# Performance work log

Hardware: AMD Instinct MI355X
Metric: run time of the kernel (lower is better)

Reference implementation:

```python
import jax, jax.numpy as jnp
import numpy as np

N_NODES = 50000
HIDDEN = 256
DEPTH = 6
NUM_GRAPHS = 500


def _build_graph(n):
    # 4-regular directed graph: node i -> (i+1, i-1, i+5, i-5) mod n.
    offs = np.array([1, -1, 5, -5], dtype=np.int64)
    src = np.repeat(np.arange(n, dtype=np.int64), 4)
    dst = (src + np.tile(offs, n)) % n
    # incoming edge ids of node u (edge id = 4*src + offset_index)
    u = np.arange(n, dtype=np.int64)
    incoming = np.stack([4 * ((u - 1) % n) + 0,
                         4 * ((u + 1) % n) + 1,
                         4 * ((u - 5) % n) + 2,
                         4 * ((u + 5) % n) + 3], axis=1)  # [n,4]
    E = 4 * n
    pred = incoming[src]           # [E,4] candidate line-graph predecessors of edge e
    pred_src = pred // 4           # source node of each predecessor edge
    keep = pred_src != dst[:, None]  # drop backtracking edge (exactly 1 per row)
    lg_src = pred[keep]                                   # [3E]
    lg_dst = np.repeat(np.arange(E, dtype=np.int64), 4)[keep.ravel()]  # [3E]
    return src, dst, lg_src, lg_dst


def setup_inputs() -> dict:
    key = jax.random.key(0)
    ks = jax.random.split(key, 8)
    n, H = N_NODES, HIDDEN
    E = 4 * n
    _, dst, lg_src, lg_dst = _build_graph(n)
    graph_ids = np.arange(n, dtype=np.int64) // (n // NUM_GRAPHS)
    s = 0.02  # small weight scale keeps relu message passing stable over DEPTH iters
    return {
        "x_nodes": jax.random.normal(ks[0], (n, 35), jnp.float32),
        "x_edges": jax.random.normal(ks[1], (E, 40), jnp.float32),
        "t_m": jax.random.normal(ks[2], (E, H), jnp.float32) * 0.1,
        "W_i": jax.random.normal(ks[3], (40, H), jnp.float32) * s,
        "W_h": jax.random.normal(ks[4], (H, H), jnp.float32) * s,
        "W_o": jax.random.normal(ks[5], (35 + H, H), jnp.float32) * s,
        "b_o": jax.random.normal(ks[6], (H,), jnp.float32) * s,
        "edge_dst": jnp.asarray(dst, jnp.int32),
        "lg_src": jnp.asarray(lg_src, jnp.int32),
        "lg_dst": jnp.asarray(lg_dst, jnp.int32),
        "graph_ids": jnp.asarray(graph_ids, jnp.int32),
        "num_graphs": NUM_GRAPHS,
    }


def reference(x_nodes, x_edges, t_m, W_i, W_h, W_o, b_o,
              edge_dst, lg_src, lg_dst, graph_ids, num_graphs):
    E = x_edges.shape[0]
    n = x_nodes.shape[0]
    binput = x_edges @ W_i                       # W_i has no bias
    g_m = jax.nn.relu(binput)                    # [E,H] per-edge message
    # tree-message aggregation over line graph is constant across depth iters
    t_agg = jax.ops.segment_sum(t_m[lg_src], lg_dst, num_segments=E)
    for _ in range(DEPTH - 1):
        g_agg = jax.ops.segment_sum(g_m[lg_src], lg_dst, num_segments=E)
        g_m = jax.nn.relu(binput + (g_agg + t_agg) @ W_h)
    # edge -> dst-node aggregation (copy_e + sum)
    nei1 = jax.ops.segment_sum(g_m, edge_dst, num_segments=n)
    nei2 = jax.ops.segment_sum(t_m, edge_dst, num_segments=n)
    ainput = jnp.concatenate([x_nodes, nei1 + nei2], axis=1)  # [n, 35+H]
    atom_hiddens = jax.nn.relu(ainput @ W_o + b_o)
    # dgl.mean_nodes: per-graph mean of node features
    sums = jax.ops.segment_sum(atom_hiddens, graph_ids, num_segments=num_graphs)
    counts = jax.ops.segment_sum(jnp.ones((n, 1), atom_hiddens.dtype), graph_ids,
                                 num_segments=num_graphs)
    return sums / counts
```

## Files before the change

### kernel.cpp

```cpp
#include <hip/hip_runtime.h>


#define H 256

typedef __attribute__((ext_vector_type(4))) float f32x4;
typedef __attribute__((ext_vector_type(8))) short bf16x8;

#define MFMA(a, b, c) __builtin_amdgcn_mfma_f32_16x16x32_bf16((a), (b), (c), 0, 0, 0)

__device__ __forceinline__ float bf2f(ushort u) {
  union { unsigned int i; float f; } v; v.i = ((unsigned int)u) << 16; return v.f;
}
__device__ __forceinline__ ushort f2bf(float f) {
  union { float f; unsigned int i; } v; v.f = f;
  unsigned int i = v.i;
  i += 0x7fffu + ((i >> 16) & 1u);
  return (ushort)(i >> 16);
}

union AFrag { bf16x8 v; ushort u[8]; };

__device__ __forceinline__ int edge_delta(int o) {
  return ((o & 2) ? 5 : 1) * ((o & 1) ? -1 : 1);
}

__device__ __forceinline__ int phi(int L) {
  return (L & ~31) | (((L >> 2) & 1) << 4) | (((L >> 3) & 3) << 2) | (L & 3);
}

__global__ __launch_bounds__(256) void prep_weights_kernel(
    const float* __restrict__ Wh, const float* __restrict__ Wi, const float* __restrict__ Wo,
    ushort* __restrict__ WhF, ushort* __restrict__ WiT,
    ushort* __restrict__ WoT1, ushort* __restrict__ WoT2) {
  const int nn = blockIdx.x;
  const int t = threadIdx.x;
  const int w = phi(nn);
  const int nfg = w >> 4, l15w = w & 15;
  const int ks = t >> 5, kg = (t >> 3) & 3, i = t & 7;
  WhF[((nfg * 8 + ks) << 9) + ((kg << 4) + l15w) * 8 + i] = f2bf(Wh[t * H + nn]);
  WoT2[nn * H + t] = f2bf(Wo[(35 + t) * H + nn]);
  if (t < 64) {
    WiT[w * 64 + t] = (t < 40) ? f2bf(Wi[t * H + nn]) : (ushort)0;
    WoT1[nn * 64 + t] = (t < 35) ? f2bf(Wo[t * H + nn]) : (ushort)0;
  }
}

__global__ __launch_bounds__(256) void sum_tm_kernel(
    const float* __restrict__ t_m, ushort* __restrict__ t3, ushort* __restrict__ t4,
    int n, int useT4) {
  const int idx = blockIdx.x * 256 + threadIdx.x;
  const int s = idx >> 5;
  if (s >= n) return;
  const int cg = (idx & 31) * 8;
  int im1 = s - 1; if (im1 < 0) im1 += n;
  int ip1 = s + 1; if (ip1 >= n) ip1 -= n;
  int im5 = s - 5; if (im5 < 0) im5 += n;
  int ip5 = s + 5; if (ip5 >= n) ip5 -= n;
  const size_t e0 = (size_t)(4 * im1 + 0) * H + cg;
  const size_t e1 = (size_t)(4 * ip1 + 1) * H + cg;
  const size_t e2 = (size_t)(4 * im5 + 2) * H + cg;
  const size_t e3 = (size_t)(4 * ip5 + 3) * H + cg;
  f32x4 v0a = *(const f32x4*)(t_m + e0), v0b = *(const f32x4*)(t_m + e0 + 4);
  f32x4 v1a = *(const f32x4*)(t_m + e1), v1b = *(const f32x4*)(t_m + e1 + 4);
  f32x4 v2a = *(const f32x4*)(t_m + e2), v2b = *(const f32x4*)(t_m + e2 + 4);
  f32x4 v3a = *(const f32x4*)(t_m + e3), v3b = *(const f32x4*)(t_m + e3 + 4);
  f32x4 Sa = v0a + v1a + v2a + v3a;
  f32x4 Sb = v0b + v1b + v2b + v3b;
  f32x4 ra[4] = {Sa - v1a, Sa - v0a, Sa - v3a, Sa - v2a};
  f32x4 rb[4] = {Sb - v1b, Sb - v0b, Sb - v3b, Sb - v2b};
#pragma unroll
  for (int o = 0; o < 4; ++o) {
    AFrag a;
#pragma unroll
    for (int i = 0; i < 4; ++i) { a.u[i] = f2bf(ra[o][i]); a.u[4 + i] = f2bf(rb[o][i]); }
    *(bf16x8*)(t3 + (size_t)(4 * s + o) * H + cg) = a.v;
  }
  if (useT4) {
    AFrag a;
#pragma unroll
    for (int i = 0; i < 4; ++i) { a.u[i] = f2bf(Sa[i]); a.u[4 + i] = f2bf(Sb[i]); }
    *(bf16x8*)(t4 + (size_t)s * H + cg) = a.v;
  }
}

__global__ __launch_bounds__(1024, 8) void prologue_kernel(
    const float* __restrict__ x_edges, const ushort* __restrict__ t3,
    const ushort* __restrict__ WhF, const ushort* __restrict__ WiT,
    ushort* __restrict__ tb, ushort* __restrict__ g0P, int E, int n) {
  extern __shared__ ushort lds[];
  const int tid = threadIdx.x;
  const int wid = tid >> 6, lane = tid & 63, l15 = lane & 15, kg = lane >> 4;
  const int ch = blockIdx.x & 1;
  const int colbase = ch << 7;

  {
    const bf16x8* src = (const bf16x8*)(WhF) + ch * 4096;
    bf16x8* dstl = (bf16x8*)lds;
#pragma unroll
    for (int j = 0; j < 4; ++j) dstl[tid + j * 1024] = src[tid + j * 1024];
  }
  __syncthreads();

  const int row0 = ((blockIdx.x >> 1) << 8) + wid * 16;
  if (row0 >= E) return;
  const int r = row0 + l15;

  const float* xp = x_edges + (size_t)r * 40;
  f32x4 xa0 = *(const f32x4*)(xp + kg * 8);
  f32x4 xa1 = *(const f32x4*)(xp + kg * 8 + 4);
  f32x4 xb0, xb1;
  if (kg == 0) { xb0 = *(const f32x4*)(xp + 32); xb1 = *(const f32x4*)(xp + 36); }

  f32x4 acc[8];
#pragma unroll
  for (int i = 0; i < 8; ++i) acc[i] = (f32x4){0.f, 0.f, 0.f, 0.f};

  AFrag bx0, bx1;
#pragma unroll
  for (int i = 0; i < 4; ++i) { bx0.u[i] = f2bf(xa0[i]); bx0.u[4 + i] = f2bf(xa1[i]); }
  if (kg == 0) {
#pragma unroll
    for (int i = 0; i < 4; ++i) { bx1.u[i] = f2bf(xb0[i]); bx1.u[4 + i] = f2bf(xb1[i]); }
  } else {
#pragma unroll
    for (int i = 0; i < 8; ++i) bx1.u[i] = 0;
  }
#pragma unroll
  for (int nf = 0; nf < 8; ++nf) {
    const int w = colbase + nf * 16 + l15;
    bf16x8 a0 = *(const bf16x8*)(WiT + w * 64 + kg * 8);
    acc[nf] = MFMA(a0, bx0.v, acc[nf]);
    bf16x8 a1 = *(const bf16x8*)(WiT + w * 64 + 32 + kg * 8);
    acc[nf] = MFMA(a1, bx1.v, acc[nf]);
  }

  const ushort* t3r = t3 + (size_t)r * H + kg * 8;
  bf16x8 av0 = *(const bf16x8*)(t3r);
  bf16x8 av1 = *(const bf16x8*)(t3r + 32);

  const int s_ = r >> 2, o_ = r & 3;
  int d_ = s_ + edge_delta(o_);
  if (d_ < 0) d_ += n; else if (d_ >= n) d_ -= n;
  ushort* gout = g0P + (size_t)(4 * d_ + o_) * H + colbase + kg * 8;
#pragma unroll
  for (int tt = 0; tt < 4; ++tt) {
    AFrag pk;
#pragma unroll
    for (int i = 0; i < 4; ++i) {
      pk.u[i]     = f2bf(fmaxf(acc[2 * tt][i], 0.f));
      pk.u[4 + i] = f2bf(fmaxf(acc[2 * tt + 1][i], 0.f));
    }
    *(bf16x8*)(gout + tt * 32) = pk.v;
  }

#pragma unroll
  for (int ks = 0; ks < 8; ++ks) {
    bf16x8 av2;
    if (ks < 6) av2 = *(const bf16x8*)(t3r + (ks + 2) * 32);
#pragma unroll
    for (int nf = 0; nf < 8; ++nf) {
      bf16x8 a = *(const bf16x8*)(lds + ((nf * 8 + ks) << 9) + (lane << 3));
      acc[nf] = MFMA(a, av0, acc[nf]);
    }
    av0 = av1; av1 = av2;
  }

  ushort* tbp = tb + (size_t)r * H + colbase + kg * 8;
#pragma unroll
  for (int tt = 0; tt < 4; ++tt) {
    AFrag pk;
#pragma unroll
    for (int i = 0; i < 4; ++i) {
      pk.u[i]     = f2bf(acc[2 * tt][i]);
      pk.u[4 + i] = f2bf(acc[2 * tt + 1][i]);
    }
    *(bf16x8*)(tbp + tt * 32) = pk.v;
  }
}

__global__ __launch_bounds__(1024, 8) void mp_iter_kernel(
    const ushort* __restrict__ gOldP, const ushort* __restrict__ tb,
    const ushort* __restrict__ WhF, ushort* __restrict__ gNewP, int E, int n) {
  extern __shared__ ushort lds[];
  const int tid = threadIdx.x;
  const int wid = tid >> 6, lane = tid & 63, l15 = lane & 15, kg = lane >> 4;
  const int ch = blockIdx.x & 1;
  const int colbase = ch << 7;

  {
    const bf16x8* src = (const bf16x8*)(WhF) + ch * 4096;
    bf16x8* dstl = (bf16x8*)lds;
#pragma unroll
    for (int j = 0; j < 4; ++j) dstl[tid + j * 1024] = src[tid + j * 1024];
  }
  __syncthreads();

  const int row0 = ((blockIdx.x >> 1) << 8) + wid * 16;
  if (row0 >= E) return;
  const int r = row0 + l15;

  const ushort* gr = gOldP + (size_t)r * H + kg * 8;
  bf16x8 av0 = *(const bf16x8*)(gr);
  bf16x8 av1 = *(const bf16x8*)(gr + 32);

  f32x4 acc[8];
#pragma unroll
  for (int i = 0; i < 8; ++i) acc[i] = (f32x4){0.f, 0.f, 0.f, 0.f};

#pragma unroll
  for (int ks = 0; ks < 8; ++ks) {
    bf16x8 av2;
    if (ks < 6) av2 = *(const bf16x8*)(gr + (ks + 2) * 32);
#pragma unroll
    for (int nf = 0; nf < 8; ++nf) {
      bf16x8 a = *(const bf16x8*)(lds + ((nf * 8 + ks) << 9) + (lane << 3));
      acc[nf] = MFMA(a, av0, acc[nf]);
    }
    av0 = av1; av1 = av2;
  }

  bf16x8 tbv[4];
  const ushort* tbp = tb + (size_t)r * H + colbase + kg * 8;
#pragma unroll
  for (int tt = 0; tt < 4; ++tt) tbv[tt] = *(const bf16x8*)(tbp + tt * 32);

  const int s = r >> 2, o = r & 3;
  int d = s + edge_delta(o);
  if (d < 0) d += n; else if (d >= n) d -= n;
  ushort* gout = gNewP + (size_t)(4 * d + o) * H + colbase + kg * 8;
#pragma unroll
  for (int tt = 0; tt < 4; ++tt) {
    AFrag pk;
#pragma unroll
    for (int i = 0; i < 4; ++i) {
      const float G0 = acc[2 * tt][i];
      const float G1 = acc[2 * tt + 1][i];
      const float t0 = G0 + __shfl_xor(G0, 2);
      const float S0 = t0 + __shfl_xor(t0, 1);
      const float t1 = G1 + __shfl_xor(G1, 2);
      const float S1 = t1 + __shfl_xor(t1, 1);
      const float d0 = __shfl_xor(G0, 1);
      const float d1 = __shfl_xor(G1, 1);
      const float v0 = bf2f((ushort)tbv[tt][i])     + (S0 - d0);
      const float v1 = bf2f((ushort)tbv[tt][4 + i]) + (S1 - d1);
      pk.u[i]     = f2bf(fmaxf(v0, 0.f));
      pk.u[4 + i] = f2bf(fmaxf(v1, 0.f));
    }
    *(bf16x8*)(gout + tt * 32) = pk.v;
  }
}

__global__ __launch_bounds__(256) void readout_kernel(
    const float* __restrict__ x_nodes, const float* __restrict__ t_m,
    const ushort* __restrict__ gP, const ushort* __restrict__ t4,
    const float* __restrict__ b_o,
    const ushort* __restrict__ WoT1, const ushort* __restrict__ WoT2,
    float* __restrict__ out, int n, int npg, int useT4) {
  const int gidx = blockIdx.x;
  const int wid = threadIdx.x >> 6;
  const int lane = threadIdx.x & 63;
  const int l15 = lane & 15;
  const int kg = lane >> 4;
  const int u0 = gidx * npg;

  __shared__ float red[H];

  f32x4 acc[2][16];
#pragma unroll
  for (int m = 0; m < 2; ++m)
#pragma unroll
    for (int i = 0; i < 16; ++i) acc[m][i] = (f32x4){0.f, 0.f, 0.f, 0.f};

  int uu[2]; bool mv[2]; int inc[2][4];
#pragma unroll
  for (int m = 0; m < 2; ++m) {
    const int mf = wid * 2 + m;
    const int rl = mf * 16 + l15;
    mv[m] = rl < npg;
    const int u = u0 + rl;
    uu[m] = u;
    if (mv[m]) {
      inc[m][0] = 4 * ((u - 1 + n) % n);
      inc[m][1] = 4 * ((u + 1) % n) + 1;
      inc[m][2] = 4 * ((u - 5 + n) % n) + 2;
      inc[m][3] = 4 * ((u + 5) % n) + 3;
    } else {
      inc[m][0] = inc[m][1] = inc[m][2] = inc[m][3] = 0;
    }
  }

#pragma unroll
  for (int ks = 0; ks < 2; ++ks) {
    const int k = ks * 32 + kg * 8;
#pragma unroll
    for (int m = 0; m < 2; ++m) {
      AFrag a;
#pragma unroll
      for (int i = 0; i < 8; ++i) {
        const int kk = k + i;
        a.u[i] = (mv[m] && kk < 35) ? f2bf(x_nodes[(size_t)uu[m] * 35 + kk]) : (ushort)0;
      }
#pragma unroll
      for (int nf = 0; nf < 16; ++nf) {
        bf16x8 b = *(const bf16x8*)(WoT1 + (nf * 16 + l15) * 64 + k);
        acc[m][nf] = MFMA(a.v, b, acc[m][nf]);
      }
    }
  }

#pragma unroll
  for (int ks = 0; ks < 8; ++ks) {
    const int k = ks * 32 + kg * 8;
#pragma unroll
    for (int m = 0; m < 2; ++m) {
      AFrag a;
      if (mv[m]) {
        float s[8];
#pragma unroll
        for (int i = 0; i < 8; ++i) s[i] = 0.f;
        const int e4 = 4 * uu[m];
#pragma unroll
        for (int j = 0; j < 4; ++j) {
          bf16x8 gv = *(const bf16x8*)(gP + (size_t)(e4 + j) * H + k);
#pragma unroll
          for (int i = 0; i < 8; ++i) s[i] += bf2f((ushort)gv[i]);
        }
        if (useT4) {
          bf16x8 tv = *(const bf16x8*)(t4 + (size_t)uu[m] * H + k);
#pragma unroll
          for (int i = 0; i < 8; ++i) s[i] += bf2f((ushort)tv[i]);
        } else {
#pragma unroll
          for (int j = 0; j < 4; ++j) {
            const float* tp = t_m + (size_t)inc[m][j] * H + k;
            f32x4 t0 = *(const f32x4*)tp;
            f32x4 t1 = *(const f32x4*)(tp + 4);
#pragma unroll
            for (int i = 0; i < 4; ++i) { s[i] += t0[i]; s[4 + i] += t1[i]; }
          }
        }
#pragma unroll
        for (int i = 0; i < 8; ++i) a.u[i] = f2bf(s[i]);
      } else {
#pragma unroll
        for (int i = 0; i < 8; ++i) a.u[i] = 0;
      }
#pragma unroll
      for (int nf = 0; nf < 16; ++nf) {
        bf16x8 b = *(const bf16x8*)(WoT2 + (nf * 16 + l15) * H + k);
        acc[m][nf] = MFMA(a.v, b, acc[m][nf]);
      }
    }
  }

  red[threadIdx.x] = 0.f;
  __syncthreads();

#pragma unroll
  for (int nf = 0; nf < 16; ++nf) {
    const int col = nf * 16 + l15;
    const float bias = b_o[col];
    float cs = 0.f;
#pragma unroll
    for (int m = 0; m < 2; ++m) {
#pragma unroll
      for (int j = 0; j < 4; ++j) {
        const int rr = (wid * 2 + m) * 16 + kg * 4 + j;
        if (rr < npg) cs += fmaxf(acc[m][nf][j] + bias, 0.f);
      }
    }
    cs += __shfl_xor(cs, 16);
    cs += __shfl_xor(cs, 32);
    if (kg == 0) atomicAdd(&red[col], cs);
  }
  __syncthreads();
  out[(size_t)gidx * H + threadIdx.x] = red[threadIdx.x] * (1.0f / (float)npg);
}

extern "C" void kernel_launch(void* const* d_in, const int* in_sizes, int n_in,
                              void* d_out, int out_size, void* d_ws, size_t ws_size,
                              hipStream_t stream) {
  const float* x_nodes = (const float*)d_in[0];
  const float* x_edges = (const float*)d_in[1];
  const float* t_m     = (const float*)d_in[2];
  const float* W_i     = (const float*)d_in[3];
  const float* W_h     = (const float*)d_in[4];
  const float* W_o     = (const float*)d_in[5];
  const float* b_o     = (const float*)d_in[6];
  (void)n_in;

  const int n = in_sizes[0] / 35;
  const int E = in_sizes[1] / 40;
  const int num_graphs = out_size / H;
  const int npg = n / num_graphs;

  char* ws = (char*)d_ws;
  ushort* WhF  = (ushort*)(ws);
  ushort* WiT  = (ushort*)(ws + 131072);
  ushort* WoT1 = (ushort*)(ws + 164 * 1024);
  ushort* WoT2 = (ushort*)(ws + 200 * 1024);
  size_t off = 336 * 1024;
  const size_t gbytes = (size_t)E * H * 2;
  ushort* tb = (ushort*)(ws + off); off += gbytes;
  ushort* gA = (ushort*)(ws + off); off += gbytes;
  ushort* gB = (ushort*)(ws + off); off += gbytes;
  ushort* t3 = gB;
  const size_t t4bytes = (size_t)n * H * 2;
  const int useT4 = (ws_size >= off + t4bytes) ? 1 : 0;
  ushort* t4 = (ushort*)(ws + off);

  const int nch = (E + 255) >> 8;

  prep_weights_kernel<<<256, 256, 0, stream>>>(W_h, W_i, W_o, WhF, WiT, WoT1, WoT2);
  sum_tm_kernel<<<(n * 32 + 255) / 256, 256, 0, stream>>>(t_m, t3, t4, n, useT4);
  prologue_kernel<<<2 * nch, 1024, 65536, stream>>>(x_edges, t3, WhF, WiT, tb, gA, E, n);

  ushort* src = gA;
  ushort* dst = gB;
  for (int it = 0; it < 5; ++it) {
    mp_iter_kernel<<<2 * nch, 1024, 65536, stream>>>(src, tb, WhF, dst, E, n);
    ushort* tmp = src; src = dst; dst = tmp;
  }

  readout_kernel<<<num_graphs, 256, 0, stream>>>(x_nodes, t_m, src, t4, b_o, WoT1, WoT2,
                                                 (float*)d_out, n, npg, useT4);
}
```

Baseline: 747.5 us.

## Store edge message buffers in MFMA fragment-tiled layout for contiguous wave loads

Changes the global layout of the per-edge bf16 buffers (t3, tb, g ping-pong buffers) and W_i from row-major to 16-row by 32-column fragment tiles. Each wave's 64 lanes now read or write one contiguous 1 KiB chunk per K-step instead of 16 rows strided by 512 bytes. This is meant to improve memory coalescing in the prologue and message-passing kernels. The readout and the scatter writes are adapted to the tiled indexing, and the scatter stores stay partly scattered.

```diff
diff --git a/kernel.cpp b/kernel.cpp
--- a/kernel.cpp
+++ b/kernel.cpp
@@ -30,7 +30,7 @@
 
 __global__ __launch_bounds__(256) void prep_weights_kernel(
     const float* __restrict__ Wh, const float* __restrict__ Wi, const float* __restrict__ Wo,
-    ushort* __restrict__ WhF, ushort* __restrict__ WiT,
+    ushort* __restrict__ WhF, ushort* __restrict__ WiTF,
     ushort* __restrict__ WoT1, ushort* __restrict__ WoT2) {
   const int nn = blockIdx.x;
   const int t = threadIdx.x;
@@ -40,7 +40,8 @@
   WhF[((nfg * 8 + ks) << 9) + ((kg << 4) + l15w) * 8 + i] = f2bf(Wh[t * H + nn]);
   WoT2[nn * H + t] = f2bf(Wo[(35 + t) * H + nn]);
   if (t < 64) {
-    WiT[w * 64 + t] = (t < 40) ? f2bf(Wi[t * H + nn]) : (ushort)0;
+    WiTF[((nfg * 2 + ks) << 9) + ((kg << 4) + l15w) * 8 + i] =
+        (t < 40) ? f2bf(Wi[t * H + nn]) : (ushort)0;
     WoT1[nn * 64 + t] = (t < 35) ? f2bf(Wo[t * H + nn]) : (ushort)0;
   }
 }
@@ -68,12 +69,15 @@
   f32x4 Sb = v0b + v1b + v2b + v3b;
   f32x4 ra[4] = {Sa - v1a, Sa - v0a, Sa - v3a, Sa - v2a};
   f32x4 rb[4] = {Sb - v1b, Sb - v0b, Sb - v3b, Sb - v2b};
+  const int cgs = cg >> 5;
+  const int cgk = (cg >> 3) & 3;
 #pragma unroll
   for (int o = 0; o < 4; ++o) {
     AFrag a;
 #pragma unroll
     for (int i = 0; i < 4; ++i) { a.u[i] = f2bf(ra[o][i]); a.u[4 + i] = f2bf(rb[o][i]); }
-    *(bf16x8*)(t3 + (size_t)(4 * s + o) * H + cg) = a.v;
+    const int e = 4 * s + o;
+    *(bf16x8*)(t3 + (((size_t)(e >> 4)) << 12) + (cgs << 9) + (((cgk << 4) + (e & 15)) << 3)) = a.v;
   }
   if (useT4) {
     AFrag a;
@@ -85,13 +89,12 @@
 
 __global__ __launch_bounds__(1024, 8) void prologue_kernel(
     const float* __restrict__ x_edges, const ushort* __restrict__ t3,
-    const ushort* __restrict__ WhF, const ushort* __restrict__ WiT,
+    const ushort* __restrict__ WhF, const ushort* __restrict__ WiTF,
     ushort* __restrict__ tb, ushort* __restrict__ g0P, int E, int n) {
   extern __shared__ ushort lds[];
   const int tid = threadIdx.x;
   const int wid = tid >> 6, lane = tid & 63, l15 = lane & 15, kg = lane >> 4;
   const int ch = blockIdx.x & 1;
-  const int colbase = ch << 7;
 
   {
     const bf16x8* src = (const bf16x8*)(WhF) + ch * 4096;
@@ -104,6 +107,7 @@
   const int row0 = ((blockIdx.x >> 1) << 8) + wid * 16;
   if (row0 >= E) return;
   const int r = row0 + l15;
+  const size_t blkoff = ((size_t)(row0 >> 4)) << 12;
 
   const float* xp = x_edges + (size_t)r * 40;
   f32x4 xa0 = *(const f32x4*)(xp + kg * 8);
@@ -111,6 +115,10 @@
   f32x4 xb0, xb1;
   if (kg == 0) { xb0 = *(const f32x4*)(xp + 32); xb1 = *(const f32x4*)(xp + 36); }
 
+  const ushort* t3r = t3 + blkoff + lane * 8;
+  bf16x8 av0 = *(const bf16x8*)(t3r);
+  bf16x8 av1 = *(const bf16x8*)(t3r + 512);
+
   f32x4 acc[8];
 #pragma unroll
   for (int i = 0; i < 8; ++i) acc[i] = (f32x4){0.f, 0.f, 0.f, 0.f};
@@ -127,21 +135,18 @@
   }
 #pragma unroll
   for (int nf = 0; nf < 8; ++nf) {
-    const int w = colbase + nf * 16 + l15;
-    bf16x8 a0 = *(const bf16x8*)(WiT + w * 64 + kg * 8);
+    bf16x8 a0 = *(const bf16x8*)(WiTF + (((ch * 8 + nf) * 2 + 0) << 9) + lane * 8);
     acc[nf] = MFMA(a0, bx0.v, acc[nf]);
-    bf16x8 a1 = *(const bf16x8*)(WiT + w * 64 + 32 + kg * 8);
+    bf16x8 a1 = *(const bf16x8*)(WiTF + (((ch * 8 + nf) * 2 + 1) << 9) + lane * 8);
     acc[nf] = MFMA(a1, bx1.v, acc[nf]);
   }
-
-  const ushort* t3r = t3 + (size_t)r * H + kg * 8;
-  bf16x8 av0 = *(const bf16x8*)(t3r);
-  bf16x8 av1 = *(const bf16x8*)(t3r + 32);
 
   const int s_ = r >> 2, o_ = r & 3;
   int d_ = s_ + edge_delta(o_);
   if (d_ < 0) d_ += n; else if (d_ >= n) d_ -= n;
-  ushort* gout = g0P + (size_t)(4 * d_ + o_) * H + colbase + kg * 8;
+  const int dd = 4 * d_ + o_;
+  ushort* gout = g0P + (((size_t)(dd >> 4)) << 12) + ((size_t)(ch * 4) << 9)
+               + (((kg << 4) + (dd & 15)) << 3);
 #pragma unroll
   for (int tt = 0; tt < 4; ++tt) {
     AFrag pk;
@@ -150,13 +155,13 @@
       pk.u[i]     = f2bf(fmaxf(acc[2 * tt][i], 0.f));
       pk.u[4 + i] = f2bf(fmaxf(acc[2 * tt + 1][i], 0.f));
     }
-    *(bf16x8*)(gout + tt * 32) = pk.v;
+    *(bf16x8*)(gout + (tt << 9)) = pk.v;
   }
 
 #pragma unroll
   for (int ks = 0; ks < 8; ++ks) {
     bf16x8 av2;
-    if (ks < 6) av2 = *(const bf16x8*)(t3r + (ks + 2) * 32);
+    if (ks < 6) av2 = *(const bf16x8*)(t3r + (ks + 2) * 512);
 #pragma unroll
     for (int nf = 0; nf < 8; ++nf) {
       bf16x8 a = *(const bf16x8*)(lds + ((nf * 8 + ks) << 9) + (lane << 3));
@@ -165,7 +170,7 @@
     av0 = av1; av1 = av2;
   }
 
-  ushort* tbp = tb + (size_t)r * H + colbase + kg * 8;
+  ushort* tbp = tb + blkoff + ((size_t)(ch * 4) << 9) + lane * 8;
 #pragma unroll
   for (int tt = 0; tt < 4; ++tt) {
     AFrag pk;
@@ -174,7 +179,7 @@
       pk.u[i]     = f2bf(acc[2 * tt][i]);
       pk.u[4 + i] = f2bf(acc[2 * tt + 1][i]);
     }
-    *(bf16x8*)(tbp + tt * 32) = pk.v;
+    *(bf16x8*)(tbp + (tt << 9)) = pk.v;
   }
 }
 
@@ -185,7 +190,6 @@
   const int tid = threadIdx.x;
   const int wid = tid >> 6, lane = tid & 63, l15 = lane & 15, kg = lane >> 4;
   const int ch = blockIdx.x & 1;
-  const int colbase = ch << 7;
 
   {
     const bf16x8* src = (const bf16x8*)(WhF) + ch * 4096;
@@ -198,10 +202,11 @@
   const int row0 = ((blockIdx.x >> 1) << 8) + wid * 16;
   if (row0 >= E) return;
   const int r = row0 + l15;
-
-  const ushort* gr = gOldP + (size_t)r * H + kg * 8;
+  const size_t blkoff = ((size_t)(row0 >> 4)) << 12;
+
+  const ushort* gr = gOldP + blkoff + lane * 8;
   bf16x8 av0 = *(const bf16x8*)(gr);
-  bf16x8 av1 = *(const bf16x8*)(gr + 32);
+  bf16x8 av1 = *(const bf16x8*)(gr + 512);
 
   f32x4 acc[8];
 #pragma unroll
@@ -210,7 +215,7 @@
 #pragma unroll
   for (int ks = 0; ks < 8; ++ks) {
     bf16x8 av2;
-    if (ks < 6) av2 = *(const bf16x8*)(gr + (ks + 2) * 32);
+    if (ks < 6) av2 = *(const bf16x8*)(gr + (ks + 2) * 512);
 #pragma unroll
     for (int nf = 0; nf < 8; ++nf) {
       bf16x8 a = *(const bf16x8*)(lds + ((nf * 8 + ks) << 9) + (lane << 3));
@@ -220,14 +225,16 @@
   }
 
   bf16x8 tbv[4];
-  const ushort* tbp = tb + (size_t)r * H + colbase + kg * 8;
-#pragma unroll
-  for (int tt = 0; tt < 4; ++tt) tbv[tt] = *(const bf16x8*)(tbp + tt * 32);
+  const ushort* tbp = tb + blkoff + ((size_t)(ch * 4) << 9) + lane * 8;
+#pragma unroll
+  for (int tt = 0; tt < 4; ++tt) tbv[tt] = *(const bf16x8*)(tbp + (tt << 9));
 
   const int s = r >> 2, o = r & 3;
   int d = s + edge_delta(o);
   if (d < 0) d += n; else if (d >= n) d -= n;
-  ushort* gout = gNewP + (size_t)(4 * d + o) * H + colbase + kg * 8;
+  const int dd = 4 * d + o;
+  ushort* gout = gNewP + (((size_t)(dd >> 4)) << 12) + ((size_t)(ch * 4) << 9)
+               + (((kg << 4) + (dd & 15)) << 3);
 #pragma unroll
   for (int tt = 0; tt < 4; ++tt) {
     AFrag pk;
@@ -246,7 +253,7 @@
       pk.u[i]     = f2bf(fmaxf(v0, 0.f));
       pk.u[4 + i] = f2bf(fmaxf(v1, 0.f));
     }
-    *(bf16x8*)(gout + tt * 32) = pk.v;
+    *(bf16x8*)(gout + (tt << 9)) = pk.v;
   }
 }
 
@@ -321,7 +328,10 @@
         const int e4 = 4 * uu[m];
 #pragma unroll
         for (int j = 0; j < 4; ++j) {
-          bf16x8 gv = *(const bf16x8*)(gP + (size_t)(e4 + j) * H + k);
+          const int e = e4 + j;
+          const ushort* gp = gP + (((size_t)(e >> 4)) << 12) + ((size_t)ks << 9)
+                           + (((kg << 4) + (e & 15)) << 3);
+          bf16x8 gv = *(const bf16x8*)gp;
 #pragma unroll
           for (int i = 0; i < 8; ++i) s[i] += bf2f((ushort)gv[i]);
         }
@@ -396,7 +406,7 @@
 
   char* ws = (char*)d_ws;
   ushort* WhF  = (ushort*)(ws);
-  ushort* WiT  = (ushort*)(ws + 131072);
+  ushort* WiTF = (ushort*)(ws + 131072);
   ushort* WoT1 = (ushort*)(ws + 164 * 1024);
   ushort* WoT2 = (ushort*)(ws + 200 * 1024);
   size_t off = 336 * 1024;
@@ -411,9 +421,9 @@
 
   const int nch = (E + 255) >> 8;
 
-  prep_weights_kernel<<<256, 256, 0, stream>>>(W_h, W_i, W_o, WhF, WiT, WoT1, WoT2);
+  prep_weights_kernel<<<256, 256, 0, stream>>>(W_h, W_i, W_o, WhF, WiTF, WoT1, WoT2);
   sum_tm_kernel<<<(n * 32 + 255) / 256, 256, 0, stream>>>(t_m, t3, t4, n, useT4);
-  prologue_kernel<<<2 * nch, 1024, 65536, stream>>>(x_edges, t3, WhF, WiT, tb, gA, E, n);
+  prologue_kernel<<<2 * nch, 1024, 65536, stream>>>(x_edges, t3, WhF, WiTF, tb, gA, E, n);
 
   ushort* src = gA;
   ushort* dst = gB;
```

New measurement: 776.4 us. +3.9%, slower.
